# Performance work log

Hardware: AMD Instinct MI355X
Metric: run time of the kernel (lower is better)

Reference implementation:

```python
import jax, jax.numpy as jnp
import numpy as np

jax.config.update("jax_enable_x64", True)  # torch lfilter runs in double precision

SR = 24000
RES_SIZE = 64
R_MIN, R_MAX = 0.9999, 0.99999
B, T = 4, 120000


def setup_inputs() -> dict:
    # Probe coefficients (fixed buffers, computed exactly as in Probe.__init__)
    theta_min = 2 * np.pi * 10.0 / SR
    theta_max = 2 * np.pi * 100.0 / SR
    theta = np.exp(np.linspace(np.log(theta_min), np.log(theta_max), RES_SIZE))
    radii = np.linspace(R_MIN, R_MAX, RES_SIZE)
    a1 = -2.0 * radii * np.cos(theta)          # [C]
    a2 = radii ** 2                             # [C]
    b0 = (1.0 - radii) * 0.5                    # [C]

    # Tank mixing weight: orthogonal init, shape [out=64, in=128] (rows orthonormal)
    rng = np.random.default_rng(1337)
    q, _ = np.linalg.qr(rng.standard_normal((2 * RES_SIZE, RES_SIZE)))  # [128,64], orthonormal cols
    W = q.T.astype(np.float32)                  # [64,128]

    key = jax.random.key(0)
    k1, k2 = jax.random.split(key)
    pred = jax.random.normal(k1, (B, 1, T), dtype=jnp.float32)
    target = jax.random.normal(k2, (B, 1, T), dtype=jnp.float32)
    return {
        "pred": pred,
        "target": target,
        "a1": jnp.asarray(a1, jnp.float64),
        "a2": jnp.asarray(a2, jnp.float64),
        "b0": jnp.asarray(b0, jnp.float64),
        "W": jnp.asarray(W, jnp.float32),
    }


def _biquad_bank(x, a1, a2, b0):
    """Biquad filter bank. x: [N, T] float64; coeffs: [C]. Returns [N, C, T].
    y[t] = b0*x[t] - a1*y[t-1] - a2*y[t-2]  (a0 = 1, b1 = b2 = 0, clamp=False)
    """
    n = x.shape[0]
    c = a1.shape[0]

    def step(carry, xt):
        y1, y2 = carry  # each [N, C]
        y = b0[None, :] * xt[:, None] - a1[None, :] * y1 - a2[None, :] * y2
        return (y, y1), y

    init = (jnp.zeros((n, c), x.dtype), jnp.zeros((n, c), x.dtype))
    _, ys = jax.lax.scan(step, init, x.T)      # [T, N, C]
    return jnp.transpose(ys, (1, 2, 0))        # [N, C, T]


def _probe(x, a1, a2, b0):
    """x: [B,1,T] float -> [B, 2C, T] float32 (fwd state ++ bwd state)."""
    xs = x[:, 0, :].astype(jnp.float64)        # [B, T]
    # run forward-time and reversed-time filters in one batched scan
    both = jnp.concatenate([xs, xs[:, ::-1]], axis=0)       # [2B, T]
    ys = _biquad_bank(both, a1, a2, b0)                      # [2B, C, T]
    nb = xs.shape[0]
    fwd_state = ys[:nb]                                      # [B, C, T]
    bwd_state = ys[nb:][:, :, ::-1]                          # [B, C, T] (flipped back)
    return jnp.concatenate([fwd_state, bwd_state], axis=1).astype(jnp.float32)


def _tank(x, W):
    """x: [B, 2C, T], W: [C, 2C] -> tanh(W @ x): [B, C, T]."""
    return jnp.tanh(jnp.einsum("bct,oc->bot", x, W))


def reference(pred, target, a1, a2, b0, W):
    t = pred.shape[-1]
    margin = t // 3
    p_emb = _tank(_probe(pred, a1, a2, b0), W)    # [B, C, T]
    t_emb = _tank(_probe(target, a1, a2, b0), W)  # [B, C, T]
    p_valid = p_emb[..., margin:t - margin]
    t_valid = t_emb[..., margin:t - margin]
    return jnp.mean(jnp.abs(p_valid - t_valid))
```

## Files before the change

kernel.cpp:

```cpp
#include <hip/hip_runtime.h>

#define T_LEN 120000
#define LBLK 160
#define PBLK 750
#define PB_USED 500
#define SEG_LEN 25
#define NSEG_USED 20
#define CCH 32
#define NCHUNK 5
#define BATCH 4
#define K0 250
#define NKV 250
#define DENOM 20480000.0
#define YSTR 130

typedef _Float16 half8 __attribute__((ext_vector_type(8)));
typedef float f32x4 __attribute__((ext_vector_type(4)));

__device__ __forceinline__ float fast_tanh(float x) {
  float e = __expf(2.0f * x);
  return 1.0f - 2.0f / (e + 1.0f);
}

__device__ __forceinline__ bool coeffs_are_f64(const void* a2p) {
  double probe = *(const double*)a2p;
  return probe > 0.9 && probe < 1.0;
}
__device__ __forceinline__ double coeff_d(const void* p, bool f64, int ch) {
  return f64 ? ((const double*)p)[ch] : (double)((const float*)p)[ch];
}

__device__ __forceinline__ void mat_pow(double A1, double A2, int e,
                                        double& r00, double& r01,
                                        double& r10, double& r11) {
  double m00 = -A1, m01 = -A2, m10 = 1.0, m11 = 0.0;
  r00 = 1.0; r01 = 0.0; r10 = 0.0; r11 = 1.0;
  while (e) {
    if (e & 1) {
      double t00 = r00 * m00 + r01 * m10, t01 = r00 * m01 + r01 * m11;
      double t10 = r10 * m00 + r11 * m10, t11 = r10 * m01 + r11 * m11;
      r00 = t00; r01 = t01; r10 = t10; r11 = t11;
    }
    e >>= 1;
    if (e) {
      double t00 = m00 * m00 + m01 * m10, t01 = m00 * m01 + m01 * m11;
      double t10 = m10 * m00 + m11 * m10, t11 = m10 * m01 + m11 * m11;
      m00 = t00; m01 = t01; m10 = t10; m11 = t11;
    }
  }
}

__global__ __launch_bounds__(256) void pass1(
    const float* __restrict__ pred, const float* __restrict__ tgt,
    const void* a1p, const void* a2p, const void* b0p,
    double* __restrict__ fbuf, double* __restrict__ wsum)
{
  if ((blockIdx.x | blockIdx.y) == 0 && threadIdx.x == 0) {
    wsum[0] = 0.0;
    ((unsigned int*)(wsum + 1))[0] = 0u;
  }
  int k = blockIdx.x;
  int g = threadIdx.x >> 6, lane = threadIdx.x & 63;
  int gu = __builtin_amdgcn_readfirstlane(g);
  int r = blockIdx.y * 4 + gu;
  int i = r >> 3, d = (r >> 2) & 1, b = r & 3;
  const float* sig = (i ? tgt : pred) + b * T_LEN;
  __shared__ float xs[4][LBLK];
  int base = k * LBLK;
  for (int j = lane; j < LBLK; j += 64)
    xs[gu][j] = d ? sig[T_LEN - 1 - (base + j)] : sig[base + j];
  __syncthreads();
  int ch = lane;
  bool f64 = coeffs_are_f64(a2p);
  float A1 = (float)coeff_d(a1p, f64, ch);
  float A2 = (float)coeff_d(a2p, f64, ch);
  float B0 = (float)coeff_d(b0p, f64, ch);
  float y1 = 0.0f, y2 = 0.0f;
  for (int j = 0; j < LBLK; ++j) {
    float y = fmaf(-A1, y1, fmaf(-A2, y2, B0 * xs[gu][j]));
    y2 = y1; y1 = y;
  }
  int s = r * 64 + ch;
  ((double2*)fbuf)[(size_t)k * 1024 + s] = make_double2((double)y1, (double)y2);
}

__global__ __launch_bounds__(64) void pass2a(
    const void* a1p, const void* a2p,
    const double* __restrict__ fbuf, double* __restrict__ sbuf,
    double* __restrict__ atab)
{
  int seg = blockIdx.x >> 4;
  int s = ((blockIdx.x & 15) << 6) + threadIdx.x;
  int ch = s & 63;
  bool f64 = coeffs_are_f64(a2p);
  double r00, r01, r10, r11;
  mat_pow(coeff_d(a1p, f64, ch), coeff_d(a2p, f64, ch), LBLK, r00, r01, r10, r11);
  const double2* fb = (const double2*)fbuf;
  double y1 = 0.0, y2 = 0.0;
  for (int jj = 0; jj < SEG_LEN / 5; ++jj) {
    size_t kb = (size_t)(seg * SEG_LEN + jj * 5) * 1024 + s;
    double2 f0 = fb[kb], f1 = fb[kb + 1024], f2 = fb[kb + 2048],
            f3 = fb[kb + 3072], f4 = fb[kb + 4096];
    double n1, n2;
    n1 = r00*y1 + r01*y2 + f0.x; n2 = r10*y1 + r11*y2 + f0.y; y1=n1; y2=n2;
    n1 = r00*y1 + r01*y2 + f1.x; n2 = r10*y1 + r11*y2 + f1.y; y1=n1; y2=n2;
    n1 = r00*y1 + r01*y2 + f2.x; n2 = r10*y1 + r11*y2 + f2.y; y1=n1; y2=n2;
    n1 = r00*y1 + r01*y2 + f3.x; n2 = r10*y1 + r11*y2 + f3.y; y1=n1; y2=n2;
    n1 = r00*y1 + r01*y2 + f4.x; n2 = r10*y1 + r11*y2 + f4.y; y1=n1; y2=n2;
  }
  ((double2*)sbuf)[(size_t)seg * 1024 + s] = make_double2(y1, y2);

  if (blockIdx.x == 0) {
    double p00 = 1.0, p01 = 0.0, p10 = 0.0, p11 = 1.0;
    double b00 = r00, b01 = r01, b10 = r10, b11 = r11;
    int e = SEG_LEN;
    while (e) {
      if (e & 1) {
        double t00 = p00*b00 + p01*b10, t01 = p00*b01 + p01*b11;
        double t10 = p10*b00 + p11*b10, t11 = p10*b01 + p11*b11;
        p00 = t00; p01 = t01; p10 = t10; p11 = t11;
      }
      e >>= 1;
      if (e) {
        double t00 = b00*b00 + b01*b10, t01 = b00*b01 + b01*b11;
        double t10 = b10*b00 + b11*b10, t11 = b10*b01 + b11*b11;
        b00 = t00; b01 = t01; b10 = t10; b11 = t11;
      }
    }
    double* ap = atab + ch * 8;
    ap[0] = r00; ap[1] = r01; ap[2] = r10; ap[3] = r11;
    ap[4] = p00; ap[5] = p01; ap[6] = p10; ap[7] = p11;
  }
}

__global__ __launch_bounds__(256, 4) void pass3(
    const float* __restrict__ pred, const float* __restrict__ tgt,
    const void* a1p, const void* a2p, const void* b0p,
    const float* __restrict__ W, const double* __restrict__ fbuf,
    const double* __restrict__ sbuf, const double* __restrict__ atab,
    double* __restrict__ wsum, float* __restrict__ out)
{
  int k = K0 + blockIdx.x;
  int b = blockIdx.y;
  int tid = threadIdx.x;
  __shared__ __align__(16) _Float16 ys[2][64 * YSTR];
  __shared__ float red[4];

  int g = tid >> 6, lane = tid & 63;
  int gu = __builtin_amdgcn_readfirstlane(g);
  int iu = gu >> 1, du = gu & 1;
  int ch = lane;
  int n0 = gu * 16;
  int lm = lane & 15, quad = lane >> 4;

  bool f64 = coeffs_are_f64(a2p);
  double A1d = coeff_d(a1p, f64, ch), A2d = coeff_d(a2p, f64, ch);
  double B0d = coeff_d(b0p, f64, ch);
  float A1 = (float)A1d, A2 = (float)A2d, B0 = (float)B0d;
  float IA2 = (float)(1.0 / A2d);

  const double2* ap = (const double2*)(atab + ch * 8);
  double2 ra = ap[0], rb = ap[1], qa = ap[2], qb = ap[3];
  double r00 = ra.x, r01 = ra.y, r10 = rb.x, r11 = rb.y;
  double q00 = qa.x, q01 = qa.y, q10 = qb.x, q11 = qb.y;

  int m = du ? (PBLK - k) : k;
  int seg = m / SEG_LEN, j = m - seg * SEG_LEN;
  int s = (iu * 8 + du * 4 + b) * 64 + ch;

  double y1 = 0.0, y2 = 0.0;
  const double2* sb = (const double2*)sbuf;
  #pragma unroll 1
  for (int qq = 0; qq < NSEG_USED; qq += 5) {
    double2 f[5];
    #pragma unroll
    for (int p = 0; p < 5; ++p) f[p] = sb[(size_t)(qq + p) * 1024 + s];
    #pragma unroll
    for (int p = 0; p < 5; ++p) {
      if (qq + p < seg) {
        double n1 = q00 * y1 + q01 * y2 + f[p].x;
        double n2 = q10 * y1 + q11 * y2 + f[p].y;
        y1 = n1; y2 = n2;
      }
    }
  }

  const double2* fb = (const double2*)fbuf;
  #pragma unroll 1
  for (int bb = 0; bb < 24; bb += 8) {
    double2 f[8];
    #pragma unroll
    for (int q = 0; q < 8; ++q) {
      int blk = seg * SEG_LEN + bb + q;
      if (blk >= PB_USED) blk = PB_USED - 1;
      f[q] = fb[(size_t)blk * 1024 + s];
    }
    #pragma unroll
    for (int q = 0; q < 8; ++q) {
      if (bb + q < j) {
        double n1 = r00 * y1 + r01 * y2 + f[q].x;
        double n2 = r10 * y1 + r11 * y2 + f[q].y;
        y1 = n1; y2 = n2;
      }
    }
  }
  float st0 = (float)y1, st1 = (float)y2;

  half8 wf[4][4];
  #pragma unroll
  for (int m0 = 0; m0 < 4; ++m0) {
    #pragma unroll
    for (int k0 = 0; k0 < 4; ++k0) {
      const float* wp = W + (m0 * 16 + lm) * 128 + k0 * 32 + quad * 8;
      float4 wa = *(const float4*)wp, wb = *(const float4*)(wp + 4);
      half8 h;
      h[0] = (_Float16)wa.x; h[1] = (_Float16)wa.y;
      h[2] = (_Float16)wa.z; h[3] = (_Float16)wa.w;
      h[4] = (_Float16)wb.x; h[5] = (_Float16)wb.y;
      h[6] = (_Float16)wb.z; h[7] = (_Float16)wb.w;
      wf[m0][k0] = h;
    }
  }

  const float* xp = (iu ? tgt : pred) + b * T_LEN + k * LBLK;

  float loss = 0.0f;
  for (int cc = 0; cc < NCHUNK; ++cc) {
    _Float16* yb = ys[cc & 1];
    if (du == 0) {
      #pragma unroll
      for (int tt = 0; tt < CCH; ++tt) {
        float x = xp[cc * CCH + tt];
        float y = fmaf(-A1, st0, fmaf(-A2, st1, B0 * x));
        yb[(2 * tt + iu) * YSTR + ch] = (_Float16)y;
        st1 = st0; st0 = y;
      }
    } else {
      #pragma unroll
      for (int tt = 0; tt < CCH; ++tt) {
        float x = xp[cc * CCH + tt];
        yb[(2 * tt + iu) * YSTR + 64 + ch] = (_Float16)st0;
        float ym2 = (fmaf(-A1, st1, B0 * x) - st0) * IA2;
        st0 = st1; st1 = ym2;
      }
    }
    __syncthreads();

    const _Float16* yrow = &yb[(n0 + lm) * YSTR + quad * 8];
    half8 bf0 = *(const half8*)(yrow);
    half8 bf1 = *(const half8*)(yrow + 32);
    half8 bf2 = *(const half8*)(yrow + 64);
    half8 bf3 = *(const half8*)(yrow + 96);
    #pragma unroll
    for (int m0 = 0; m0 < 4; ++m0) {
      f32x4 c = {0.f, 0.f, 0.f, 0.f};
      c = __builtin_amdgcn_mfma_f32_16x16x32_f16(wf[m0][0], bf0, c, 0, 0, 0);
      c = __builtin_amdgcn_mfma_f32_16x16x32_f16(wf[m0][1], bf1, c, 0, 0, 0);
      c = __builtin_amdgcn_mfma_f32_16x16x32_f16(wf[m0][2], bf2, c, 0, 0, 0);
      c = __builtin_amdgcn_mfma_f32_16x16x32_f16(wf[m0][3], bf3, c, 0, 0, 0);
      #pragma unroll
      for (int r = 0; r < 4; ++r) {
        float vv = fast_tanh(c[r]);
        float p = __shfl_xor(vv, 1);
        loss += fabsf(vv - p);
      }
    }
  }

  #pragma unroll
  for (int off = 32; off > 0; off >>= 1) loss += __shfl_down(loss, off);
  if (lane == 0) red[g] = loss;
  __syncthreads();
  if (tid == 0) {
    float blk = (red[0] + red[1]) + (red[2] + red[3]);
    atomicAdd(wsum, (double)blk);
    __threadfence();
    unsigned int n = atomicAdd((unsigned int*)(wsum + 1), 1u);
    if (n == (unsigned int)(NKV * BATCH - 1)) {
      __threadfence();
      double tot = atomicAdd(wsum, 0.0);
      out[0] = (float)(tot / DENOM);
    }
  }
}

extern "C" void kernel_launch(void* const* d_in, const int* in_sizes, int n_in,
                              void* d_out, int out_size, void* d_ws, size_t ws_size,
                              hipStream_t stream) {
  const float* pred = (const float*)d_in[0];
  const float* tgt  = (const float*)d_in[1];
  const void* a1p = d_in[2];
  const void* a2p = d_in[3];
  const void* b0p = d_in[4];
  const float* W  = (const float*)d_in[5];
  float* out = (float*)d_out;

  double* base = (double*)d_ws;
  double* wsum = base;
  double* fbuf = base + 8;
  double* sbuf = fbuf + (size_t)PB_USED * 1024 * 2;
  double* atab = sbuf + (size_t)32 * 1024 * 2;

  pass1<<<dim3(PB_USED, 4), 256, 0, stream>>>(pred, tgt, a1p, a2p, b0p,
                                              fbuf, wsum);
  pass2a<<<NSEG_USED * 16, 64, 0, stream>>>(a1p, a2p, fbuf, sbuf, atab);
  pass3<<<dim3(NKV, BATCH), 256, 0, stream>>>(pred, tgt, a1p, a2p, b0p,
                                              W, fbuf, sbuf, atab, wsum, out);
}
```

Measured before the change: 126.9 us.

## Precompute per-block initial filter states in a separate pass instead of per-block replay

```diff
diff --git a/kernel.cpp b/kernel.cpp
--- a/kernel.cpp
+++ b/kernel.cpp
@@ -6,6 +6,8 @@
 #define PB_USED 500
 #define SEG_LEN 25
 #define NSEG_USED 20
+#define SEGC0 10
+#define NSEGC 11
 #define CCH 32
 #define NCHUNK 5
 #define BATCH 4
@@ -133,11 +135,65 @@
   }
 }
 
+__global__ __launch_bounds__(64) void pass2c(
+    const double* __restrict__ fbuf, const double* __restrict__ sbuf,
+    const double* __restrict__ atab, double* __restrict__ stbuf)
+{
+  int seg = SEGC0 + (blockIdx.x >> 4);
+  int s = ((blockIdx.x & 15) << 6) + threadIdx.x;
+  int ch = s & 63;
+  const double2* ap = (const double2*)(atab + ch * 8);
+  double2 ra = ap[0], rb = ap[1], qa = ap[2], qb = ap[3];
+  double r00 = ra.x, r01 = ra.y, r10 = rb.x, r11 = rb.y;
+  double q00 = qa.x, q01 = qa.y, q10 = qb.x, q11 = qb.y;
+
+  double y1 = 0.0, y2 = 0.0;
+  const double2* sb = (const double2*)sbuf;
+  #pragma unroll 1
+  for (int qq = 0; qq < NSEG_USED; qq += 5) {
+    double2 f[5];
+    #pragma unroll
+    for (int p = 0; p < 5; ++p) f[p] = sb[(size_t)(qq + p) * 1024 + s];
+    #pragma unroll
+    for (int p = 0; p < 5; ++p) {
+      if (qq + p < seg) {
+        double n1 = q00 * y1 + q01 * y2 + f[p].x;
+        double n2 = q10 * y1 + q11 * y2 + f[p].y;
+        y1 = n1; y2 = n2;
+      }
+    }
+  }
+
+  const double2* fb = (const double2*)fbuf;
+  double2* st = (double2*)stbuf;
+  #pragma unroll 1
+  for (int jb = 0; jb < SEG_LEN; jb += 5) {
+    double2 fv[5];
+    #pragma unroll
+    for (int q = 0; q < 5; ++q) {
+      int m = seg * SEG_LEN + jb + q;
+      int mc = m < PB_USED ? m : PB_USED - 1;
+      fv[q] = fb[(size_t)mc * 1024 + s];
+    }
+    #pragma unroll
+    for (int q = 0; q < 5; ++q) {
+      int m = seg * SEG_LEN + jb + q;
+      if (m <= K0 + NKV) {
+        st[(size_t)(m - K0) * 1024 + s] = make_double2(y1, y2);
+        if (m < K0 + NKV) {
+          double n1 = r00 * y1 + r01 * y2 + fv[q].x;
+          double n2 = r10 * y1 + r11 * y2 + fv[q].y;
+          y1 = n1; y2 = n2;
+        }
+      }
+    }
+  }
+}
+
 __global__ __launch_bounds__(256, 4) void pass3(
     const float* __restrict__ pred, const float* __restrict__ tgt,
     const void* a1p, const void* a2p, const void* b0p,
-    const float* __restrict__ W, const double* __restrict__ fbuf,
-    const double* __restrict__ sbuf, const double* __restrict__ atab,
+    const float* __restrict__ W, const double* __restrict__ stbuf,
     double* __restrict__ wsum, float* __restrict__ out)
 {
   int k = K0 + blockIdx.x;
@@ -159,52 +215,10 @@
   float A1 = (float)A1d, A2 = (float)A2d, B0 = (float)B0d;
   float IA2 = (float)(1.0 / A2d);
 
-  const double2* ap = (const double2*)(atab + ch * 8);
-  double2 ra = ap[0], rb = ap[1], qa = ap[2], qb = ap[3];
-  double r00 = ra.x, r01 = ra.y, r10 = rb.x, r11 = rb.y;
-  double q00 = qa.x, q01 = qa.y, q10 = qb.x, q11 = qb.y;
-
   int m = du ? (PBLK - k) : k;
-  int seg = m / SEG_LEN, j = m - seg * SEG_LEN;
   int s = (iu * 8 + du * 4 + b) * 64 + ch;
-
-  double y1 = 0.0, y2 = 0.0;
-  const double2* sb = (const double2*)sbuf;
-  #pragma unroll 1
-  for (int qq = 0; qq < NSEG_USED; qq += 5) {
-    double2 f[5];
-    #pragma unroll
-    for (int p = 0; p < 5; ++p) f[p] = sb[(size_t)(qq + p) * 1024 + s];
-    #pragma unroll
-    for (int p = 0; p < 5; ++p) {
-      if (qq + p < seg) {
-        double n1 = q00 * y1 + q01 * y2 + f[p].x;
-        double n2 = q10 * y1 + q11 * y2 + f[p].y;
-        y1 = n1; y2 = n2;
-      }
-    }
-  }
-
-  const double2* fb = (const double2*)fbuf;
-  #pragma unroll 1
-  for (int bb = 0; bb < 24; bb += 8) {
-    double2 f[8];
-    #pragma unroll
-    for (int q = 0; q < 8; ++q) {
-      int blk = seg * SEG_LEN + bb + q;
-      if (blk >= PB_USED) blk = PB_USED - 1;
-      f[q] = fb[(size_t)blk * 1024 + s];
-    }
-    #pragma unroll
-    for (int q = 0; q < 8; ++q) {
-      if (bb + q < j) {
-        double n1 = r00 * y1 + r01 * y2 + f[q].x;
-        double n2 = r10 * y1 + r11 * y2 + f[q].y;
-        y1 = n1; y2 = n2;
-      }
-    }
-  }
-  float st0 = (float)y1, st1 = (float)y2;
+  double2 v0 = ((const double2*)stbuf)[(size_t)(m - K0) * 1024 + s];
+  float st0 = (float)v0.x, st1 = (float)v0.y;
 
   half8 wf[4][4];
   #pragma unroll
@@ -300,10 +314,12 @@
   double* fbuf = base + 8;
   double* sbuf = fbuf + (size_t)PB_USED * 1024 * 2;
   double* atab = sbuf + (size_t)32 * 1024 * 2;
+  double* stbuf = atab + 512;
 
   pass1<<<dim3(PB_USED, 4), 256, 0, stream>>>(pred, tgt, a1p, a2p, b0p,
                                               fbuf, wsum);
   pass2a<<<NSEG_USED * 16, 64, 0, stream>>>(a1p, a2p, fbuf, sbuf, atab);
+  pass2c<<<NSEGC * 16, 64, 0, stream>>>(fbuf, sbuf, atab, stbuf);
   pass3<<<dim3(NKV, BATCH), 256, 0, stream>>>(pred, tgt, a1p, a2p, b0p,
-                                              W, fbuf, sbuf, atab, wsum, out);
-}
+                                              W, stbuf, wsum, out);
+}
```

Result: no change. 128.7 us (+1.4%).
